# Kernel optimization log

Hardware: AMD Instinct MI355X
Metric: run time of the kernel (lower is better)

The kernel has to match this reference:

```python
import jax, jax.numpy as jnp
import numpy as np
import math

BIG, SMALL, HEADS, FF_MULT = 4096, 256, 4, 2
HEAD_DIM = SMALL // HEADS
FF = SMALL * FF_MULT
EPS = 1.1920929e-07  # torch.nn.RMSNorm default eps=None -> finfo(float32).eps


def rmsnorm(x, g):
    var = jnp.mean(x * x, axis=-1, keepdims=True)
    return x * jax.lax.rsqrt(var + EPS) * g


def setup_inputs() -> dict:
    key = jax.random.key(0)
    ks = jax.random.split(key, 10)
    B, T = 4, 2048
    def lin(k, out_d, in_d):
        # torch nn.Linear default init: U(-1/sqrt(in), 1/sqrt(in)), weight shape (out, in)
        lim = 1.0 / math.sqrt(in_d)
        return jax.random.uniform(k, (out_d, in_d), jnp.float32, -lim, lim)
    return {
        "x": jax.random.normal(ks[0], (B, T, BIG), jnp.float32),
        "W_down": lin(ks[1], SMALL, BIG),
        "W_up": lin(ks[2], BIG, SMALL),
        "W_qkv": lin(ks[3], 3 * SMALL, SMALL),
        "W_o": lin(ks[4], SMALL, SMALL),
        "W_gate": lin(ks[5], FF, SMALL),
        "W_upff": lin(ks[6], FF, SMALL),
        "W_downff": lin(ks[7], SMALL, FF),
        "g1": jnp.ones((SMALL,), jnp.float32),
        "g2": jnp.ones((SMALL,), jnp.float32),
    }


def reference(x, W_down, W_up, W_qkv, W_o, W_gate, W_upff, W_downff, g1, g2):
    B, T, _ = x.shape
    h = x @ W_down.T                                     # (B,T,small)
    hn = rmsnorm(h, g1)
    qkv = (hn @ W_qkv.T).reshape(B, T, 3, HEADS, HEAD_DIM)
    qkv = jnp.transpose(qkv, (2, 0, 3, 1, 4))            # (3,B,H,T,hd)
    q, k, v = qkv[0], qkv[1], qkv[2]
    scores = jnp.einsum('bhqd,bhkd->bhqk', q, k) / math.sqrt(HEAD_DIM)
    causal = jnp.tril(jnp.ones((T, T), bool))
    scores = jnp.where(causal, scores, -jnp.inf)
    attn = jax.nn.softmax(scores, axis=-1)
    out = jnp.einsum('bhqk,bhkd->bhqd', attn, v)
    out = jnp.transpose(out, (0, 2, 1, 3)).reshape(B, T, SMALL)
    h = h + out @ W_o.T
    hn = rmsnorm(h, g2)
    ff = (jax.nn.silu(hn @ W_gate.T) * (hn @ W_upff.T)) @ W_downff.T
    h = h + ff
    return h @ W_up.T                                    # (B,T,big)
```

## Files before the change

### kernel.cpp

```cpp
#include <hip/hip_runtime.h>
#include <hip/hip_bf16.h>

typedef __bf16 bf16x8 __attribute__((ext_vector_type(8)));
typedef __bf16 bf16x4 __attribute__((ext_vector_type(4)));
typedef float f32x4 __attribute__((ext_vector_type(4)));

#define MFMA_BF16(a, b, c) __builtin_amdgcn_mfma_f32_16x16x32_bf16((a), (b), (c), 0, 0, 0)

__device__ __forceinline__ void g2lds16(void* lds, const void* g) {
  __builtin_amdgcn_global_load_lds(
      (const __attribute__((address_space(1))) void*)g,
      (__attribute__((address_space(3))) void*)lds, 16, 0, 0);
}

enum { EP_BF16 = 0, EP_F32 = 1, EP_ADD_F32 = 2, EP_ADD_BF16OUT = 3 };

template <int EPI, int MT, bool SPLITK = false>
__global__ __launch_bounds__(256, 4) void gemm_nt_kernel(
    const __bf16* __restrict__ A, const __bf16* __restrict__ B, const int K,
    __bf16* __restrict__ Co, float* __restrict__ Cf, const int ldc)
{
  __shared__ __align__(16) __bf16 As[2][MT * 32];
  __shared__ __align__(16) __bf16 Bs[2][128 * 32];
  const int tid = threadIdx.x;
  const int wv = tid >> 6, lane = tid & 63;
  const int r16 = lane & 15, g4 = lane >> 4;
  const int row0 = blockIdx.y * MT, col0 = blockIdx.x * 128;
  const int wr = (MT == 128) ? (wv >> 1) * 64 : 0;
  const int wc = (MT == 128) ? (wv & 1) * 64 : wv * 32;
  constexpr int NW = (MT == 128) ? 4 : 2;
  constexpr int MFR = (MT >= 64) ? 4 : 2;
  const int kz0 = SPLITK ? blockIdx.z * 1024 : 0;

  f32x4 acc[MFR][NW];
#pragma unroll
  for (int m = 0; m < MFR; ++m)
#pragma unroll
    for (int n = 0; n < NW; ++n) acc[m][n] = f32x4{0.f, 0.f, 0.f, 0.f};

  auto stage = [&](int buf, int k0) {
    if constexpr (MT == 32) {
      if (tid < 128) {
        const int u = tid, row = u >> 2, cg = ((u & 3) ^ (row & 3)) * 8;
        g2lds16(&As[buf][u * 8], A + (size_t)(row0 + row) * K + k0 + cg);
      }
    } else {
#pragma unroll
      for (int rr = 0; rr < MT / 64; ++rr) {
        const int u = rr * 256 + tid, row = u >> 2, cg = ((u & 3) ^ (row & 3)) * 8;
        g2lds16(&As[buf][u * 8], A + (size_t)(row0 + row) * K + k0 + cg);
      }
    }
#pragma unroll
    for (int rr = 0; rr < 2; ++rr) {
      const int u = rr * 256 + tid, row = u >> 2, cg = ((u & 3) ^ (row & 3)) * 8;
      g2lds16(&Bs[buf][u * 8], B + (size_t)(col0 + row) * K + k0 + cg);
    }
  };

  const int nk = SPLITK ? 32 : (K >> 5);
  const int csw = (g4 ^ (r16 & 3)) * 8;
  int cur = 0;
  stage(0, kz0);
  __syncthreads();

  for (int t = 0; t < nk; ++t) {
    if (t + 1 < nk) stage(cur ^ 1, kz0 + (t + 1) * 32);
    bf16x8 af[MFR], bfr[NW];
#pragma unroll
    for (int m = 0; m < MFR; ++m)
      af[m] = *(const bf16x8*)&As[cur][(wr + m * 16 + r16) * 32 + csw];
#pragma unroll
    for (int n = 0; n < NW; ++n)
      bfr[n] = *(const bf16x8*)&Bs[cur][(wc + n * 16 + r16) * 32 + csw];
#pragma unroll
    for (int m = 0; m < MFR; ++m)
#pragma unroll
      for (int n = 0; n < NW; ++n)
        acc[m][n] = MFMA_BF16(af[m], bfr[n], acc[m][n]);
    __syncthreads();
    cur ^= 1;
  }

  const size_t zoff = SPLITK ? (size_t)blockIdx.z * 2097152 : 0;
#pragma unroll
  for (int m = 0; m < MFR; ++m)
#pragma unroll
    for (int n = 0; n < NW; ++n)
#pragma unroll
      for (int r = 0; r < 4; ++r) {
        const int row = row0 + wr + m * 16 + g4 * 4 + r;
        const int col = col0 + wc + n * 16 + r16;
        const size_t idx = (size_t)row * ldc + col;
        const float v = acc[m][n][r];
        if constexpr (EPI == EP_BF16) Co[zoff + idx] = (__bf16)v;
        else if constexpr (EPI == EP_F32) __builtin_nontemporal_store(v, &Cf[idx]);
        else if constexpr (EPI == EP_ADD_F32) Cf[idx] += v;
        else Co[idx] = (__bf16)(Cf[idx] + v);
      }
}

__global__ __launch_bounds__(256, 2) void gemm_gu_kernel(
    const __bf16* __restrict__ A, const __bf16* __restrict__ Bg,
    const __bf16* __restrict__ Bu, __bf16* __restrict__ ffmid)
{
  __shared__ __align__(16) __bf16 As[2][64 * 32];
  __shared__ __align__(16) __bf16 Bgs[2][128 * 32];
  __shared__ __align__(16) __bf16 Bus[2][128 * 32];
  const int tid = threadIdx.x;
  const int wv = tid >> 6, lane = tid & 63;
  const int r16 = lane & 15, g4 = lane >> 4;
  const int row0 = blockIdx.y * 64, col0 = blockIdx.x * 128;
  const int wc = wv * 32;

  f32x4 accG[4][2], accU[4][2];
#pragma unroll
  for (int m = 0; m < 4; ++m)
#pragma unroll
    for (int n = 0; n < 2; ++n) {
      accG[m][n] = f32x4{0.f, 0.f, 0.f, 0.f};
      accU[m][n] = f32x4{0.f, 0.f, 0.f, 0.f};
    }

  auto stage = [&](int buf, int k0) {
    {
      const int u = tid, row = u >> 2, cg = ((u & 3) ^ (row & 3)) * 8;
      g2lds16(&As[buf][u * 8], A + (size_t)(row0 + row) * 256 + k0 + cg);
    }
#pragma unroll
    for (int rr = 0; rr < 2; ++rr) {
      const int u = rr * 256 + tid, row = u >> 2, cg = ((u & 3) ^ (row & 3)) * 8;
      g2lds16(&Bgs[buf][u * 8], Bg + (size_t)(col0 + row) * 256 + k0 + cg);
      g2lds16(&Bus[buf][u * 8], Bu + (size_t)(col0 + row) * 256 + k0 + cg);
    }
  };

  const int csw = (g4 ^ (r16 & 3)) * 8;
  int cur = 0;
  stage(0, 0);
  __syncthreads();

  for (int t = 0; t < 8; ++t) {
    if (t + 1 < 8) stage(cur ^ 1, (t + 1) * 32);
    bf16x8 af[4], bg[2], bu[2];
#pragma unroll
    for (int m = 0; m < 4; ++m)
      af[m] = *(const bf16x8*)&As[cur][(m * 16 + r16) * 32 + csw];
#pragma unroll
    for (int n = 0; n < 2; ++n) {
      bg[n] = *(const bf16x8*)&Bgs[cur][(wc + n * 16 + r16) * 32 + csw];
      bu[n] = *(const bf16x8*)&Bus[cur][(wc + n * 16 + r16) * 32 + csw];
    }
#pragma unroll
    for (int m = 0; m < 4; ++m)
#pragma unroll
      for (int n = 0; n < 2; ++n) {
        accG[m][n] = MFMA_BF16(af[m], bg[n], accG[m][n]);
        accU[m][n] = MFMA_BF16(af[m], bu[n], accU[m][n]);
      }
    __syncthreads();
    cur ^= 1;
  }

#pragma unroll
  for (int m = 0; m < 4; ++m)
#pragma unroll
    for (int n = 0; n < 2; ++n)
#pragma unroll
      for (int r = 0; r < 4; ++r) {
        const int row = row0 + m * 16 + g4 * 4 + r;
        const int col = col0 + wc + n * 16 + r16;
        const float g = accG[m][n][r];
        const float u = accU[m][n][r];
        ffmid[(size_t)row * 512 + col] = (__bf16)((g / (1.f + __expf(-g))) * u);
      }
}

__global__ __launch_bounds__(256, 2) void gemm_wo_kernel(
    const __bf16* __restrict__ opart, const float* __restrict__ lpart,
    const __bf16* __restrict__ B, float* __restrict__ Cf)
{
  __shared__ __align__(16) __bf16 As[2][32 * 32];
  __shared__ __align__(16) __bf16 Bs[2][128 * 32];
  const int tid = threadIdx.x;
  const int wv = tid >> 6, lane = tid & 63;
  const int r16 = lane & 15, g4 = lane >> 4;
  const int row0 = blockIdx.y * 32, col0 = blockIdx.x * 128;
  const int wc = wv * 32;

  f32x4 acc[2][2];
#pragma unroll
  for (int m = 0; m < 2; ++m)
#pragma unroll
    for (int n = 0; n < 2; ++n) acc[m][n] = f32x4{0.f, 0.f, 0.f, 0.f};

  const int arow = tid >> 2;
  const int R = row0 + (arow & 31);
  const int b = R >> 11, rr_ = R & 2047;
  const int qb = rr_ >> 6, rloc = rr_ & 63;
  const int cgrp = ((tid & 3) ^ (arow & 3)) * 8;

  auto stageA = [&](int buf, int t) {
    if (tid < 128) {
      const int hh = t >> 1;
      const int dbase = (t & 1) * 32 + cgrp;
      const size_t pb = ((size_t)((b * 4 + hh) * 32 + qb)) * 2;
      const bf16x8 o0 = *(const bf16x8*)(opart + pb * 4096 + rloc * 64 + dbase);
      const bf16x8 o1 = *(const bf16x8*)(opart + (pb + 1) * 4096 + rloc * 64 + dbase);
      const float inv = 1.f / (lpart[pb * 64 + rloc] + lpart[(pb + 1) * 64 + rloc]);
      bf16x8 w;
#pragma unroll
      for (int j = 0; j < 8; ++j) w[j] = (__bf16)(((float)o0[j] + (float)o1[j]) * inv);
      *(bf16x8*)&As[buf][tid * 8] = w;
    }
  };
  auto stageB = [&](int buf, int k0) {
#pragma unroll
    for (int rr = 0; rr < 2; ++rr) {
      const int u = rr * 256 + tid, row = u >> 2, cg = ((u & 3) ^ (row & 3)) * 8;
      g2lds16(&Bs[buf][u * 8], B + (size_t)(col0 + row) * 256 + k0 + cg);
    }
  };

  const int csw = (g4 ^ (r16 & 3)) * 8;
  int cur = 0;
  stageA(0, 0);
  stageB(0, 0);
  __syncthreads();

  for (int t = 0; t < 8; ++t) {
    if (t + 1 < 8) { stageA(cur ^ 1, t + 1); stageB(cur ^ 1, (t + 1) * 32); }
    bf16x8 af[2], bfr[2];
#pragma unroll
    for (int m = 0; m < 2; ++m)
      af[m] = *(const bf16x8*)&As[cur][(m * 16 + r16) * 32 + csw];
#pragma unroll
    for (int n = 0; n < 2; ++n)
      bfr[n] = *(const bf16x8*)&Bs[cur][(wc + n * 16 + r16) * 32 + csw];
#pragma unroll
    for (int m = 0; m < 2; ++m)
#pragma unroll
      for (int n = 0; n < 2; ++n)
        acc[m][n] = MFMA_BF16(af[m], bfr[n], acc[m][n]);
    __syncthreads();
    cur ^= 1;
  }

#pragma unroll
  for (int m = 0; m < 2; ++m)
#pragma unroll
    for (int n = 0; n < 2; ++n)
#pragma unroll
      for (int r = 0; r < 4; ++r) {
        const int row = row0 + m * 16 + g4 * 4 + r;
        const int col = col0 + wc + n * 16 + r16;
        Cf[(size_t)row * 256 + col] += acc[m][n][r];
      }
}

__global__ void rmsnorm_reduce_kernel(const __bf16* __restrict__ part, const float* __restrict__ g,
                                      float* __restrict__ h, __bf16* __restrict__ out)
{
  const int wv = threadIdx.x >> 6, lane = threadIdx.x & 63;
  const size_t row = (size_t)blockIdx.x * 4 + wv;
  const size_t i = row * 256 + lane * 4;
  f32x4 v = {0.f, 0.f, 0.f, 0.f};
#pragma unroll
  for (int z = 0; z < 4; ++z) {
    const bf16x4 p = *(const bf16x4*)(part + (size_t)z * 2097152 + i);
#pragma unroll
    for (int j = 0; j < 4; ++j) v[j] += (float)p[j];
  }
  *(f32x4*)(h + i) = v;
  float s = v[0] * v[0] + v[1] * v[1] + v[2] * v[2] + v[3] * v[3];
#pragma unroll
  for (int off = 1; off < 64; off <<= 1) s += __shfl_xor(s, off);
  const float scale = rsqrtf(s * (1.f / 256.f) + 1.1920929e-07f);
  const f32x4 gv = *(const f32x4*)(g + lane * 4);
  bf16x4 o;
#pragma unroll
  for (int j = 0; j < 4; ++j) o[j] = (__bf16)(v[j] * scale * gv[j]);
  *(bf16x4*)(out + i) = o;
}

__global__ void rmsnorm_kernel(const float* __restrict__ h, const float* __restrict__ g,
                               __bf16* __restrict__ out)
{
  const int wv = threadIdx.x >> 6, lane = threadIdx.x & 63;
  const size_t row = (size_t)blockIdx.x * 4 + wv;
  const f32x4 v = *(const f32x4*)(h + row * 256 + lane * 4);
  float s = v[0] * v[0] + v[1] * v[1] + v[2] * v[2] + v[3] * v[3];
#pragma unroll
  for (int off = 1; off < 64; off <<= 1) s += __shfl_xor(s, off);
  const float scale = rsqrtf(s * (1.f / 256.f) + 1.1920929e-07f);
  const f32x4 gv = *(const f32x4*)(g + lane * 4);
  bf16x4 o;
#pragma unroll
  for (int j = 0; j < 4; ++j) o[j] = (__bf16)(v[j] * scale * gv[j]);
  *(bf16x4*)(out + row * 256 + lane * 4) = o;
}

struct CvtPack { const float* s[8]; __bf16* d[8]; int n[8]; };
__global__ void cvt_all_kernel(CvtPack p)
{
  int i = (blockIdx.x * 256 + threadIdx.x) * 4;
#pragma unroll
  for (int k = 0; k < 8; ++k) {
    if (i < p.n[k]) {
      const f32x4 v = *(const f32x4*)(p.s[k] + i);
      bf16x4 o;
#pragma unroll
      for (int j = 0; j < 4; ++j) o[j] = (__bf16)v[j];
      *(bf16x4*)(p.d[k] + i) = o;
      return;
    }
    i -= p.n[k];
  }
}

__global__ __launch_bounds__(256, 4) void attn_kernel(
    const __bf16* __restrict__ qkv, __bf16* __restrict__ opart, float* __restrict__ lpart)
{
  const int bh = blockIdx.x;
  const int by = blockIdx.y;
  const int qb = (by < 16) ? (31 - by) : (by - 16);
  const int z = blockIdx.z;
  const int b = bh >> 2, hh = bh & 3;
  const int tid = threadIdx.x, wv = tid >> 6, lane = tid & 63;
  const int r16 = lane & 15, g4 = lane >> 4;
  const __bf16* base = qkv + (size_t)b * 2048 * 768;
  const int q0 = qb * 64;

  __shared__ __align__(16) __bf16 Ks[2][64 * 64];
  __shared__ __align__(16) __bf16 Vt[64 * 72];
  __shared__ __align__(16) __bf16 Ps[4][16 * 72];

  bf16x8 qf[2];
  {
    const __bf16* qrow = base + (size_t)(q0 + wv * 16 + r16) * 768 + hh * 64;
    qf[0] = *(const bf16x8*)(qrow + g4 * 8);
    qf[1] = *(const bf16x8*)(qrow + 32 + g4 * 8);
  }

  f32x4 oacc[4];
#pragma unroll
  for (int t = 0; t < 4; ++t) oacc[t] = f32x4{0.f, 0.f, 0.f, 0.f};
  float lsum[4] = {0.f, 0.f, 0.f, 0.f};

  auto stageK = [&](int buf, int kv0) {
#pragma unroll
    for (int rr = 0; rr < 2; ++rr) {
      const int u = rr * 256 + tid;
      const int kv = u >> 3, c = u & 7;
      g2lds16(&Ks[buf][u * 8],
              base + (size_t)(kv0 + kv) * 768 + 256 + hh * 64 + ((c ^ (kv & 7)) * 8));
    }
  };
  const int vrow = tid >> 2, vdg = (tid & 3) * 16;
  const int va_ = vrow >> 3, vb_ = vrow & 7;

  bf16x8 v0r, v1r;
  auto loadV = [&](int kv0) {
    const __bf16* vsrc = base + (size_t)(kv0 + vrow) * 768 + 512 + hh * 64 + vdg;
    v0r = *(const bf16x8*)vsrc;
    v1r = *(const bf16x8*)(vsrc + 8);
  };
  auto writeVt = [&]() {
#pragma unroll
    for (int i = 0; i < 8; ++i) {
      int d = vdg + i;
      Vt[d * 72 + ((va_ ^ (d >> 3)) << 3) + vb_] = v0r[i];
      d = vdg + 8 + i;
      Vt[d * 72 + ((va_ ^ (d >> 3)) << 3) + vb_] = v1r[i];
    }
  };

  int c = z, cur = 0;
  const bool any = (c <= qb);
  if (any) { stageK(0, c * 64); loadV(c * 64); }
  __syncthreads();
  if (any) writeVt();
  __syncthreads();

  while (c <= qb) {
    const int nxt = c + 2;
    if (nxt <= qb) { stageK(cur ^ 1, nxt * 64); loadV(nxt * 64); }

    f32x4 sacc[4];
#pragma unroll
    for (int t = 0; t < 4; ++t) sacc[t] = f32x4{0.f, 0.f, 0.f, 0.f};
#pragma unroll
    for (int t = 0; t < 4; ++t)
#pragma unroll
      for (int kk = 0; kk < 2; ++kk) {
        const bf16x8 kf = *(const bf16x8*)
            &Ks[cur][(t * 16 + r16) * 64 + (((kk * 4 + g4) ^ (r16 & 7)) * 8)];
        sacc[t] = MFMA_BF16(qf[kk], kf, sacc[t]);
      }

    const bool diag = (c == qb);
#pragma unroll
    for (int t = 0; t < 4; ++t)
#pragma unroll
      for (int r = 0; r < 4; ++r) {
        float p = __expf(sacc[t][r] * 0.125f);
        if (diag && (t * 16 + r16 > wv * 16 + g4 * 4 + r)) p = 0.f;
        lsum[r] += p;
        Ps[wv][(g4 * 4 + r) * 72 + t * 16 + r16] = (__bf16)p;
      }
    bf16x8 pa[2];
    pa[0] = *(const bf16x8*)&Ps[wv][r16 * 72 + g4 * 8];
    pa[1] = *(const bf16x8*)&Ps[wv][r16 * 72 + 32 + g4 * 8];

#pragma unroll
    for (int t2 = 0; t2 < 4; ++t2)
#pragma unroll
      for (int kk = 0; kk < 2; ++kk) {
        const int d = t2 * 16 + r16;
        const bf16x8 vf = *(const bf16x8*)
            &Vt[d * 72 + (((kk * 4 + g4) ^ (d >> 3)) * 8)];
        oacc[t2] = MFMA_BF16(pa[kk], vf, oacc[t2]);
      }

    __syncthreads();
    if (nxt <= qb) writeVt();
    __syncthreads();
    c = nxt;
    cur ^= 1;
  }

#pragma unroll
  for (int r = 0; r < 4; ++r) {
    lsum[r] += __shfl_xor(lsum[r], 1);
    lsum[r] += __shfl_xor(lsum[r], 2);
    lsum[r] += __shfl_xor(lsum[r], 4);
    lsum[r] += __shfl_xor(lsum[r], 8);
  }
  const size_t pb = (size_t)(bh * 32 + qb) * 2 + z;
  __bf16* op = opart + pb * 4096;
#pragma unroll
  for (int t2 = 0; t2 < 4; ++t2)
#pragma unroll
    for (int r = 0; r < 4; ++r)
      op[(wv * 16 + g4 * 4 + r) * 64 + t2 * 16 + r16] = (__bf16)oacc[t2][r];
  if (r16 == 0) {
    float* lp = lpart + pb * 64;
#pragma unroll
    for (int r = 0; r < 4; ++r) lp[wv * 16 + g4 * 4 + r] = lsum[r];
  }
}

extern "C" void kernel_launch(void* const* d_in, const int* in_sizes, int n_in,
                              void* d_out, int out_size, void* d_ws, size_t ws_size,
                              hipStream_t stream) {
  (void)in_sizes; (void)n_in; (void)out_size; (void)ws_size;
  const float* x     = (const float*)d_in[0];
  const float* Wdown = (const float*)d_in[1];
  const float* Wup   = (const float*)d_in[2];
  const float* Wqkv  = (const float*)d_in[3];
  const float* Wo    = (const float*)d_in[4];
  const float* Wgate = (const float*)d_in[5];
  const float* Wupff = (const float*)d_in[6];
  const float* Wdff  = (const float*)d_in[7];
  const float* g1    = (const float*)d_in[8];
  const float* g2    = (const float*)d_in[9];
  float* out = (float*)d_out;

  const size_t MB = 1 << 20;
  char* ws = (char*)d_ws;
  float*  h  = (float*)ws;
  __bf16* hn = (__bf16*)(ws + 8 * MB);
  __bf16* hb = (__bf16*)(ws + 12 * MB);
  __bf16* wb_down = (__bf16*)(ws + 16 * MB);
  __bf16* wb_up   = (__bf16*)(ws + 18 * MB);
  __bf16* wb_qkv  = (__bf16*)(ws + 20 * MB);
  __bf16* wb_o    = (__bf16*)(ws + 20 * MB + 384 * 1024);
  __bf16* wb_gate = (__bf16*)(ws + 20 * MB + 512 * 1024);
  __bf16* wb_upff = (__bf16*)(ws + 20 * MB + 768 * 1024);
  __bf16* wb_dff  = (__bf16*)(ws + 21 * MB);

  char* ob = (char*)d_out;
  __bf16* xb    = (__bf16*)(ob);
  __bf16* hpart = (__bf16*)(ob + 64 * MB);
  __bf16* qkv   = (__bf16*)(ob);
  __bf16* ffmid = (__bf16*)(ob + 12 * MB);
  __bf16* opart = (__bf16*)(ob + 36 * MB);
  float* lpart  = (float*)(ob + 53 * MB);

  CvtPack cp;
  cp.s[0] = Wdown; cp.d[0] = wb_down; cp.n[0] = 1048576;
  cp.s[1] = Wup;   cp.d[1] = wb_up;   cp.n[1] = 1048576;
  cp.s[2] = Wqkv;  cp.d[2] = wb_qkv;  cp.n[2] = 196608;
  cp.s[3] = Wo;    cp.d[3] = wb_o;    cp.n[3] = 65536;
  cp.s[4] = Wgate; cp.d[4] = wb_gate; cp.n[4] = 131072;
  cp.s[5] = Wupff; cp.d[5] = wb_upff; cp.n[5] = 131072;
  cp.s[6] = Wdff;  cp.d[6] = wb_dff;  cp.n[6] = 131072;
  cp.s[7] = x;     cp.d[7] = xb;      cp.n[7] = 33554432;
  cvt_all_kernel<<<35456, 256, 0, stream>>>(cp);

  gemm_nt_kernel<EP_BF16, 128, true><<<dim3(2, 64, 4), 256, 0, stream>>>(
      xb, wb_down, 4096, hpart, nullptr, 256);
  rmsnorm_reduce_kernel<<<2048, 256, 0, stream>>>(hpart, g1, h, hn);

  gemm_nt_kernel<EP_BF16, 64><<<dim3(6, 128), 256, 0, stream>>>(
      hn, wb_qkv, 256, qkv, nullptr, 768);
  attn_kernel<<<dim3(16, 32, 2), 256, 0, stream>>>(qkv, opart, lpart);
  gemm_wo_kernel<<<dim3(2, 256), 256, 0, stream>>>(opart, lpart, wb_o, h);
  rmsnorm_kernel<<<2048, 256, 0, stream>>>(h, g2, hn);
  gemm_gu_kernel<<<dim3(4, 128), 256, 0, stream>>>(hn, wb_gate, wb_upff, ffmid);
  gemm_nt_kernel<EP_ADD_BF16OUT, 32><<<dim3(2, 256), 256, 0, stream>>>(
      ffmid, wb_dff, 512, hb, h, 256);
  gemm_nt_kernel<EP_F32, 128><<<dim3(32, 64), 256, 0, stream>>>(
      hb, wb_up, 256, nullptr, out, 4096);
}
```

Measured before the change: 195.8 us.

## Drop attention split-K partials and fuse W_o GEMM with second RMSNorm

Attention no longer splits the key range across two blocks per query tile. Each block now walks all key tiles, normalizes by the row sum and writes the final bf16 output directly, which removes the opart/lpart partial buffers and the combine step. The W_o GEMM now covers full 256-column rows per block, so it can add the residual and compute the RMSNorm in its epilogue using a cross-wave shared-memory reduction. This removes the standalone rmsnorm kernel and a pass over h. In exchange, attention launches half as many blocks with longer causal-imbalanced work, and the W_o GEMM has fewer, larger blocks.

```diff
diff --git a/kernel.cpp b/kernel.cpp
--- a/kernel.cpp
+++ b/kernel.cpp
@@ -176,86 +176,104 @@
       }
 }
 
-__global__ __launch_bounds__(256, 2) void gemm_wo_kernel(
-    const __bf16* __restrict__ opart, const float* __restrict__ lpart,
-    const __bf16* __restrict__ B, float* __restrict__ Cf)
+__global__ __launch_bounds__(256, 2) void gemm_wo_rms_kernel(
+    const __bf16* __restrict__ A, const __bf16* __restrict__ B,
+    const float* __restrict__ g, float* __restrict__ h, __bf16* __restrict__ hn)
 {
   __shared__ __align__(16) __bf16 As[2][32 * 32];
-  __shared__ __align__(16) __bf16 Bs[2][128 * 32];
+  __shared__ __align__(16) __bf16 Bs[2][256 * 32];
+  __shared__ float rs[4][32];
   const int tid = threadIdx.x;
   const int wv = tid >> 6, lane = tid & 63;
   const int r16 = lane & 15, g4 = lane >> 4;
-  const int row0 = blockIdx.y * 32, col0 = blockIdx.x * 128;
-  const int wc = wv * 32;
-
-  f32x4 acc[2][2];
+  const int row0 = blockIdx.x * 32;
+  const int wc = wv * 64;
+
+  f32x4 acc[2][4];
 #pragma unroll
   for (int m = 0; m < 2; ++m)
 #pragma unroll
-    for (int n = 0; n < 2; ++n) acc[m][n] = f32x4{0.f, 0.f, 0.f, 0.f};
-
-  const int arow = tid >> 2;
-  const int R = row0 + (arow & 31);
-  const int b = R >> 11, rr_ = R & 2047;
-  const int qb = rr_ >> 6, rloc = rr_ & 63;
-  const int cgrp = ((tid & 3) ^ (arow & 3)) * 8;
-
-  auto stageA = [&](int buf, int t) {
+    for (int n = 0; n < 4; ++n) acc[m][n] = f32x4{0.f, 0.f, 0.f, 0.f};
+
+  auto stage = [&](int buf, int k0) {
     if (tid < 128) {
-      const int hh = t >> 1;
-      const int dbase = (t & 1) * 32 + cgrp;
-      const size_t pb = ((size_t)((b * 4 + hh) * 32 + qb)) * 2;
-      const bf16x8 o0 = *(const bf16x8*)(opart + pb * 4096 + rloc * 64 + dbase);
-      const bf16x8 o1 = *(const bf16x8*)(opart + (pb + 1) * 4096 + rloc * 64 + dbase);
-      const float inv = 1.f / (lpart[pb * 64 + rloc] + lpart[(pb + 1) * 64 + rloc]);
-      bf16x8 w;
-#pragma unroll
-      for (int j = 0; j < 8; ++j) w[j] = (__bf16)(((float)o0[j] + (float)o1[j]) * inv);
-      *(bf16x8*)&As[buf][tid * 8] = w;
-    }
-  };
-  auto stageB = [&](int buf, int k0) {
-#pragma unroll
-    for (int rr = 0; rr < 2; ++rr) {
+      const int u = tid, row = u >> 2, cg = ((u & 3) ^ (row & 3)) * 8;
+      g2lds16(&As[buf][u * 8], A + (size_t)(row0 + row) * 256 + k0 + cg);
+    }
+#pragma unroll
+    for (int rr = 0; rr < 4; ++rr) {
       const int u = rr * 256 + tid, row = u >> 2, cg = ((u & 3) ^ (row & 3)) * 8;
-      g2lds16(&Bs[buf][u * 8], B + (size_t)(col0 + row) * 256 + k0 + cg);
+      g2lds16(&Bs[buf][u * 8], B + (size_t)row * 256 + k0 + cg);
     }
   };
 
   const int csw = (g4 ^ (r16 & 3)) * 8;
   int cur = 0;
-  stageA(0, 0);
-  stageB(0, 0);
+  stage(0, 0);
   __syncthreads();
 
   for (int t = 0; t < 8; ++t) {
-    if (t + 1 < 8) { stageA(cur ^ 1, t + 1); stageB(cur ^ 1, (t + 1) * 32); }
-    bf16x8 af[2], bfr[2];
+    if (t + 1 < 8) stage(cur ^ 1, (t + 1) * 32);
+    bf16x8 af[2], bfr[4];
 #pragma unroll
     for (int m = 0; m < 2; ++m)
       af[m] = *(const bf16x8*)&As[cur][(m * 16 + r16) * 32 + csw];
 #pragma unroll
-    for (int n = 0; n < 2; ++n)
+    for (int n = 0; n < 4; ++n)
       bfr[n] = *(const bf16x8*)&Bs[cur][(wc + n * 16 + r16) * 32 + csw];
 #pragma unroll
     for (int m = 0; m < 2; ++m)
 #pragma unroll
-      for (int n = 0; n < 2; ++n)
+      for (int n = 0; n < 4; ++n)
         acc[m][n] = MFMA_BF16(af[m], bfr[n], acc[m][n]);
     __syncthreads();
     cur ^= 1;
   }
 
+  float hv[2][4][4];
 #pragma unroll
   for (int m = 0; m < 2; ++m)
 #pragma unroll
-    for (int n = 0; n < 2; ++n)
+    for (int n = 0; n < 4; ++n)
 #pragma unroll
       for (int r = 0; r < 4; ++r) {
-        const int row = row0 + m * 16 + g4 * 4 + r;
-        const int col = col0 + wc + n * 16 + r16;
-        Cf[(size_t)row * 256 + col] += acc[m][n][r];
-      }
+        const size_t idx = (size_t)(row0 + m * 16 + g4 * 4 + r) * 256 + wc + n * 16 + r16;
+        const float v = h[idx] + acc[m][n][r];
+        hv[m][n][r] = v;
+        h[idx] = v;
+      }
+
+#pragma unroll
+  for (int m = 0; m < 2; ++m)
+#pragma unroll
+    for (int r = 0; r < 4; ++r) {
+      float s = 0.f;
+#pragma unroll
+      for (int n = 0; n < 4; ++n) s += hv[m][n][r] * hv[m][n][r];
+      s += __shfl_xor(s, 1);
+      s += __shfl_xor(s, 2);
+      s += __shfl_xor(s, 4);
+      s += __shfl_xor(s, 8);
+      if (r16 == 0) rs[wv][m * 16 + g4 * 4 + r] = s;
+    }
+  __syncthreads();
+
+  float gc[4];
+#pragma unroll
+  for (int n = 0; n < 4; ++n) gc[n] = g[wc + n * 16 + r16];
+#pragma unroll
+  for (int m = 0; m < 2; ++m)
+#pragma unroll
+    for (int r = 0; r < 4; ++r) {
+      const int rl = m * 16 + g4 * 4 + r;
+      const float tot = rs[0][rl] + rs[1][rl] + rs[2][rl] + rs[3][rl];
+      const float scale = rsqrtf(tot * (1.f / 256.f) + 1.1920929e-07f);
+#pragma unroll
+      for (int n = 0; n < 4; ++n) {
+        const size_t idx = (size_t)(row0 + rl) * 256 + wc + n * 16 + r16;
+        hn[idx] = (__bf16)(hv[m][n][r] * scale * gc[n]);
+      }
+    }
 }
 
 __global__ void rmsnorm_reduce_kernel(const __bf16* __restrict__ part, const float* __restrict__ g,
@@ -283,23 +301,6 @@
   *(bf16x4*)(out + i) = o;
 }
 
-__global__ void rmsnorm_kernel(const float* __restrict__ h, const float* __restrict__ g,
-                               __bf16* __restrict__ out)
-{
-  const int wv = threadIdx.x >> 6, lane = threadIdx.x & 63;
-  const size_t row = (size_t)blockIdx.x * 4 + wv;
-  const f32x4 v = *(const f32x4*)(h + row * 256 + lane * 4);
-  float s = v[0] * v[0] + v[1] * v[1] + v[2] * v[2] + v[3] * v[3];
-#pragma unroll
-  for (int off = 1; off < 64; off <<= 1) s += __shfl_xor(s, off);
-  const float scale = rsqrtf(s * (1.f / 256.f) + 1.1920929e-07f);
-  const f32x4 gv = *(const f32x4*)(g + lane * 4);
-  bf16x4 o;
-#pragma unroll
-  for (int j = 0; j < 4; ++j) o[j] = (__bf16)(v[j] * scale * gv[j]);
-  *(bf16x4*)(out + row * 256 + lane * 4) = o;
-}
-
 struct CvtPack { const float* s[8]; __bf16* d[8]; int n[8]; };
 __global__ void cvt_all_kernel(CvtPack p)
 {
@@ -319,12 +320,11 @@
 }
 
 __global__ __launch_bounds__(256, 4) void attn_kernel(
-    const __bf16* __restrict__ qkv, __bf16* __restrict__ opart, float* __restrict__ lpart)
+    const __bf16* __restrict__ qkv, __bf16* __restrict__ ao)
 {
   const int bh = blockIdx.x;
   const int by = blockIdx.y;
   const int qb = (by < 16) ? (31 - by) : (by - 16);
-  const int z = blockIdx.z;
   const int b = bh >> 2, hh = bh & 3;
   const int tid = threadIdx.x, wv = tid >> 6, lane = tid & 63;
   const int r16 = lane & 15, g4 = lane >> 4;
@@ -375,15 +375,15 @@
     }
   };
 
-  int c = z, cur = 0;
-  const bool any = (c <= qb);
-  if (any) { stageK(0, c * 64); loadV(c * 64); }
+  int c = 0, cur = 0;
+  stageK(0, 0);
+  loadV(0);
   __syncthreads();
-  if (any) writeVt();
+  writeVt();
   __syncthreads();
 
   while (c <= qb) {
-    const int nxt = c + 2;
+    const int nxt = c + 1;
     if (nxt <= qb) { stageK(cur ^ 1, nxt * 64); loadV(nxt * 64); }
 
     f32x4 sacc[4];
@@ -436,18 +436,14 @@
     lsum[r] += __shfl_xor(lsum[r], 4);
     lsum[r] += __shfl_xor(lsum[r], 8);
   }
-  const size_t pb = (size_t)(bh * 32 + qb) * 2 + z;
-  __bf16* op = opart + pb * 4096;
 #pragma unroll
   for (int t2 = 0; t2 < 4; ++t2)
 #pragma unroll
-    for (int r = 0; r < 4; ++r)
-      op[(wv * 16 + g4 * 4 + r) * 64 + t2 * 16 + r16] = (__bf16)oacc[t2][r];
-  if (r16 == 0) {
-    float* lp = lpart + pb * 64;
-#pragma unroll
-    for (int r = 0; r < 4; ++r) lp[wv * 16 + g4 * 4 + r] = lsum[r];
-  }
+    for (int r = 0; r < 4; ++r) {
+      const int row = q0 + wv * 16 + g4 * 4 + r;
+      const int col = hh * 64 + t2 * 16 + r16;
+      ao[((size_t)b * 2048 + row) * 256 + col] = (__bf16)(oacc[t2][r] / lsum[r]);
+    }
 }
 
 extern "C" void kernel_launch(void* const* d_in, const int* in_sizes, int n_in,
@@ -484,8 +480,7 @@
   __bf16* hpart = (__bf16*)(ob + 64 * MB);
   __bf16* qkv   = (__bf16*)(ob);
   __bf16* ffmid = (__bf16*)(ob + 12 * MB);
-  __bf16* opart = (__bf16*)(ob + 36 * MB);
-  float* lpart  = (float*)(ob + 53 * MB);
+  __bf16* ao    = (__bf16*)(ob + 20 * MB);
 
   CvtPack cp;
   cp.s[0] = Wdown; cp.d[0] = wb_down; cp.n[0] = 1048576;
@@ -504,9 +499,8 @@
 
   gemm_nt_kernel<EP_BF16, 64><<<dim3(6, 128), 256, 0, stream>>>(
       hn, wb_qkv, 256, qkv, nullptr, 768);
-  attn_kernel<<<dim3(16, 32, 2), 256, 0, stream>>>(qkv, opart, lpart);
-  gemm_wo_kernel<<<dim3(2, 256), 256, 0, stream>>>(opart, lpart, wb_o, h);
-  rmsnorm_kernel<<<2048, 256, 0, stream>>>(h, g2, hn);
+  attn_kernel<<<dim3(16, 32), 256, 0, stream>>>(qkv, ao);
+  gemm_wo_rms_kernel<<<256, 256, 0, stream>>>(ao, wb_o, g2, h, hn);
   gemm_gu_kernel<<<dim3(4, 128), 256, 0, stream>>>(hn, wb_gate, wb_upff, ffmid);
   gemm_nt_kernel<EP_ADD_BF16OUT, 32><<<dim3(2, 256), 256, 0, stream>>>(
       ffmid, wb_dff, 512, hb, h, 256);
```

New measurement: 209.5 us. +7.0%, slower.
